# Kernel tuning notes

Hardware: AMD Instinct MI355X
Metric: run time of the kernel (lower is better)

Reference implementation:

```python
import jax, jax.numpy as jnp
import numpy as np

SUPPORT_FACTOR = 2.5
EPSILON = 1e-5


def setup_inputs() -> dict:
    key = jax.random.key(0)
    k1, _ = jax.random.split(key)
    # 64x64 regular particle grid on [0,1]^2 -> N = 4096 nodes
    n_side = 64
    g = jnp.linspace(0.0, 1.0, n_side, dtype=jnp.float32)
    gx, gy = jnp.meshgrid(g, g, indexing='ij')
    nodes = jnp.stack([gx.ravel(), gy.ravel()], axis=-1)  # [4096, 2]
    # B = 4096 query (collocation) points inside the same domain
    x = jax.random.uniform(k1, (4096, 2), dtype=jnp.float32)
    return {"x": x, "nodes": nodes}


def _cubic_spline(q):
    # piecewise cubic spline kernel; zero outside q > 1
    w_inner = 2.0 / 3.0 - 4.0 * q ** 2 + 4.0 * q ** 3          # q <= 0.5
    w_outer = 4.0 / 3.0 - 4.0 * q + 4.0 * q ** 2 - (4.0 / 3.0) * q ** 3  # 0.5 < q <= 1
    return jnp.where(q <= 0.5, w_inner, jnp.where(q <= 1.0, w_outer, 0.0))


def _dilation(nodes):
    # support_factor * mean nearest-neighbor spacing (replaces init-time cKDTree)
    d2 = jnp.sum((nodes[:, None, :] - nodes[None, :, :]) ** 2, axis=-1)  # [N, N]
    d2 = d2 + jnp.where(jnp.eye(nodes.shape[0], dtype=bool), jnp.inf, 0.0)
    h_avg = jnp.mean(jnp.sqrt(jnp.min(d2, axis=1)))
    return SUPPORT_FACTOR * h_avg


def reference(x, nodes):
    dilation = _dilation(nodes)
    diff = x[:, None, :] - nodes[None, :, :]          # [B, N, 2]
    dx = diff[..., 0]
    dy = diff[..., 1]
    dist = jnp.sqrt(dx ** 2 + dy ** 2 + 1e-10)        # [B, N]
    q = dist / dilation
    w = _cubic_spline(q) * (q <= 1.0)                 # support-radius mask
    ones = jnp.ones_like(dx)
    P = jnp.stack([ones, dx, dy], axis=-1)            # [B, N, 3]
    M = jnp.einsum('bni,bnj,bn->bij', P, P, w)        # [B, 3, 3] moment matrices
    M_reg = M + jnp.eye(3, dtype=x.dtype) * EPSILON
    M_inv = jnp.linalg.inv(M_reg)                     # batched 3x3 inverse
    P_w = P * w[..., None]
    b_vec = jnp.einsum('bij,bnj->bni', M_inv, P_w)    # [B, N, 3]
    phi = b_vec[..., 0]
    phi_x = -b_vec[..., 1]
    phi_y = -b_vec[..., 2]
    return (phi, phi_x, phi_y)
```

## Files before the change

### kernel.cpp

```cpp
#include <hip/hip_runtime.h>

#define N_NODES 4096
#define B_PTS   4096
#define SUPPORT_FACTOR 2.5f
#define EPSILON 1e-5f

__global__ __launch_bounds__(256) void nearest_kernel(
        const float* __restrict__ nodes, float* __restrict__ mind) {
    const int i = blockIdx.x;
    const float xi = nodes[2 * i];
    const float yi = nodes[2 * i + 1];

    const float4* nodes4 = (const float4*)nodes;
    float mind2 = 3.4e38f;
    for (int k = threadIdx.x; k < N_NODES / 2; k += 256) {
        float4 v = nodes4[k];
        float dx0 = xi - v.x, dy0 = yi - v.y;
        float dx1 = xi - v.z, dy1 = yi - v.w;
        float d20 = dx0 * dx0 + dy0 * dy0;
        float d21 = dx1 * dx1 + dy1 * dy1;
        if (2 * k != i)     mind2 = fminf(mind2, d20);
        if (2 * k + 1 != i) mind2 = fminf(mind2, d21);
    }
    #pragma unroll
    for (int off = 32; off > 0; off >>= 1)
        mind2 = fminf(mind2, __shfl_down(mind2, off, 64));

    __shared__ float sw[4];
    const int wave = threadIdx.x >> 6;
    if ((threadIdx.x & 63) == 0) sw[wave] = mind2;
    __syncthreads();
    if (threadIdx.x == 0) {
        float m = fminf(fminf(sw[0], sw[1]), fminf(sw[2], sw[3]));
        mind[i] = sqrtf(m);
    }
}

__device__ __forceinline__ float cubic_w(float q) {
    if (q <= 0.5f) return 2.0f / 3.0f + q * q * (4.0f * q - 4.0f);
    if (q <= 1.0f) return 4.0f / 3.0f + q * (-4.0f + q * (4.0f - (4.0f / 3.0f) * q));
    return 0.0f;
}

__global__ __launch_bounds__(256, 4) void rkpm_kernel(
        const float* __restrict__ x, const float* __restrict__ nodes,
        const float* __restrict__ mind, float* __restrict__ out) {
    __shared__ float sred[4][6];
    __shared__ float sbc[10];

    const int b = blockIdx.x;
    const int tid = threadIdx.x;
    const int wave = tid >> 6;
    const int lane = tid & 63;

    const float4* m4 = (const float4*)mind;
    float s = 0.f;
    #pragma unroll
    for (int k = 0; k < 4; ++k) {
        float4 v = m4[k * 256 + tid];
        s += (v.x + v.y) + (v.z + v.w);
    }
    #pragma unroll
    for (int off = 32; off > 0; off >>= 1)
        s += __shfl_down(s, off, 64);
    if (lane == 0) sred[wave][0] = s;
    __syncthreads();
    if (tid == 0) {
        float dil = (sred[0][0] + sred[1][0] + sred[2][0] + sred[3][0]) *
                    (SUPPORT_FACTOR / (float)N_NODES);
        sbc[0] = 1.0f / dil;
    }
    __syncthreads();
    const float inv_dil = sbc[0];

    const float2 xq = ((const float2*)x)[b];
    const float xb = xq.x, yb = xq.y;

    const float4* nodes4 = (const float4*)nodes;
    float wr[16], dxr[16], dyr[16];
    float m00 = 0.f, m01 = 0.f, m02 = 0.f, m11 = 0.f, m12 = 0.f, m22 = 0.f;
    #pragma unroll
    for (int kk = 0; kk < 4; ++kk) {
        float4 va = nodes4[kk * 512 + 2 * tid];
        float4 vb = nodes4[kk * 512 + 2 * tid + 1];
        #pragma unroll
        for (int c = 0; c < 4; ++c) {
            float nx = (c == 0) ? va.x : (c == 1) ? va.z : (c == 2) ? vb.x : vb.z;
            float ny = (c == 0) ? va.y : (c == 1) ? va.w : (c == 2) ? vb.y : vb.w;
            float dx = xb - nx;
            float dy = yb - ny;
            float dist = sqrtf(dx * dx + dy * dy + 1e-10f);
            float w = cubic_w(dist * inv_dil);
            const int r = kk * 4 + c;
            wr[r] = w; dxr[r] = dx; dyr[r] = dy;
            m00 += w;
            m01 += w * dx;
            m02 += w * dy;
            m11 += w * dx * dx;
            m12 += w * dx * dy;
            m22 += w * dy * dy;
        }
    }
    #pragma unroll
    for (int off = 32; off > 0; off >>= 1) {
        m00 += __shfl_down(m00, off, 64);
        m01 += __shfl_down(m01, off, 64);
        m02 += __shfl_down(m02, off, 64);
        m11 += __shfl_down(m11, off, 64);
        m12 += __shfl_down(m12, off, 64);
        m22 += __shfl_down(m22, off, 64);
    }
    if (lane == 0) {
        sred[wave][0] = m00; sred[wave][1] = m01; sred[wave][2] = m02;
        sred[wave][3] = m11; sred[wave][4] = m12; sred[wave][5] = m22;
    }
    __syncthreads();

    if (tid == 0) {
        float a  = sred[0][0] + sred[1][0] + sred[2][0] + sred[3][0] + EPSILON;
        float bb = sred[0][1] + sred[1][1] + sred[2][1] + sred[3][1];
        float c  = sred[0][2] + sred[1][2] + sred[2][2] + sred[3][2];
        float d  = sred[0][3] + sred[1][3] + sred[2][3] + sred[3][3] + EPSILON;
        float e  = sred[0][4] + sred[1][4] + sred[2][4] + sred[3][4];
        float f  = sred[0][5] + sred[1][5] + sred[2][5] + sred[3][5] + EPSILON;
        float c00 = d * f - e * e;
        float c01 = c * e - bb * f;
        float c02 = bb * e - c * d;
        float det = a * c00 + bb * c01 + c * c02;
        float idet = 1.0f / det;
        float i00 = c00 * idet;
        float i01 = c01 * idet;
        float i02 = c02 * idet;
        float i11 = (a * f - c * c) * idet;
        float i12 = (bb * c - a * e) * idet;
        float i22 = (a * d - bb * bb) * idet;
        sbc[1] = i00;  sbc[2] = i01;  sbc[3] = i02;
        sbc[4] = -i01; sbc[5] = -i11; sbc[6] = -i12;
        sbc[7] = -i02; sbc[8] = -i12; sbc[9] = -i22;
    }
    __syncthreads();

    const float i00 = sbc[1], i01 = sbc[2], i02 = sbc[3];
    const float n01 = sbc[4], n11 = sbc[5], n12 = sbc[6];
    const float n02 = sbc[7], n12b = sbc[8], n22 = sbc[9];

    const size_t BN = (size_t)B_PTS * N_NODES;
    float4* __restrict__ out_phi = (float4*)(out + (size_t)b * N_NODES);
    float4* __restrict__ out_px  = (float4*)(out + BN + (size_t)b * N_NODES);
    float4* __restrict__ out_py  = (float4*)(out + 2 * BN + (size_t)b * N_NODES);

    #pragma unroll
    for (int kk = 0; kk < 4; ++kk) {
        float4 ph, px, py;
        #pragma unroll
        for (int c = 0; c < 4; ++c) {
            const int r = kk * 4 + c;
            float w = wr[r], dx = dxr[r], dy = dyr[r];
            float vph = w * (i00 + i01 * dx + i02 * dy);
            float vpx = w * (n01 + n11 * dx + n12 * dy);
            float vpy = w * (n02 + n12b * dx + n22 * dy);
            if (c == 0)      { ph.x = vph; px.x = vpx; py.x = vpy; }
            else if (c == 1) { ph.y = vph; px.y = vpx; py.y = vpy; }
            else if (c == 2) { ph.z = vph; px.z = vpx; py.z = vpy; }
            else             { ph.w = vph; px.w = vpx; py.w = vpy; }
        }
        const int idx = kk * 256 + tid;
        out_phi[idx] = ph;
        out_px[idx]  = px;
        out_py[idx]  = py;
    }
}

extern "C" void kernel_launch(void* const* d_in, const int* in_sizes, int n_in,
                              void* d_out, int out_size, void* d_ws, size_t ws_size,
                              hipStream_t stream) {
    const float* x     = (const float*)d_in[0];
    const float* nodes = (const float*)d_in[1];
    float* out  = (float*)d_out;
    float* mind = (float*)d_ws;

    nearest_kernel<<<N_NODES, 256, 0, stream>>>(nodes, mind);
    rkpm_kernel<<<B_PTS, 256, 0, stream>>>(x, nodes, mind, out);
}
```

Measured before the change: 209.8 us.

## Exploit compact kernel support with zero-fill and sparse scatter of nonzeros

Each output row is first filled with zeros using float4 stores. Groups of four nodes are then culled by squared distance against the squared support radius, so the sqrt, spline and moment work run only for groups that can contribute. Surviving nonzero shape-function values are written with scalar scatter stores, and the register arrays that held all weights are gone. The dilation reduction moves into a single-block kernel, so the 4096 blocks no longer each re-read the whole nearest-distance buffer. The trade-off is a second pass over node positions, scalar stores that rewrite cache lines already zeroed, and one extra kernel launch.

```diff
diff --git a/kernel.cpp b/kernel.cpp
--- a/kernel.cpp
+++ b/kernel.cpp
@@ -36,69 +36,95 @@
     }
 }
 
+__global__ __launch_bounds__(256) void dil_kernel(float* __restrict__ mind) {
+    __shared__ float sw[4];
+    const int tid = threadIdx.x;
+    const float4* m4 = (const float4*)mind;
+    float s = 0.f;
+    #pragma unroll
+    for (int k = 0; k < 4; ++k) {
+        float4 v = m4[k * 256 + tid];
+        s += (v.x + v.y) + (v.z + v.w);
+    }
+    #pragma unroll
+    for (int off = 32; off > 0; off >>= 1)
+        s += __shfl_down(s, off, 64);
+    if ((tid & 63) == 0) sw[tid >> 6] = s;
+    __syncthreads();
+    if (tid == 0) {
+        float dil = (sw[0] + sw[1] + sw[2] + sw[3]) *
+                    (SUPPORT_FACTOR / (float)N_NODES);
+        mind[0] = 1.0f / dil;
+        mind[1] = dil * dil * 1.0002f + 1e-9f;
+    }
+}
+
 __device__ __forceinline__ float cubic_w(float q) {
     if (q <= 0.5f) return 2.0f / 3.0f + q * q * (4.0f * q - 4.0f);
     if (q <= 1.0f) return 4.0f / 3.0f + q * (-4.0f + q * (4.0f - (4.0f / 3.0f) * q));
     return 0.0f;
 }
 
-__global__ __launch_bounds__(256, 4) void rkpm_kernel(
+__global__ __launch_bounds__(256) void rkpm_sparse(
         const float* __restrict__ x, const float* __restrict__ nodes,
-        const float* __restrict__ mind, float* __restrict__ out) {
+        const float* __restrict__ dilp, float* __restrict__ out) {
     __shared__ float sred[4][6];
-    __shared__ float sbc[10];
+    __shared__ float sbc[9];
 
     const int b = blockIdx.x;
     const int tid = threadIdx.x;
     const int wave = tid >> 6;
     const int lane = tid & 63;
 
-    const float4* m4 = (const float4*)mind;
-    float s = 0.f;
-    #pragma unroll
-    for (int k = 0; k < 4; ++k) {
-        float4 v = m4[k * 256 + tid];
-        s += (v.x + v.y) + (v.z + v.w);
-    }
-    #pragma unroll
-    for (int off = 32; off > 0; off >>= 1)
-        s += __shfl_down(s, off, 64);
-    if (lane == 0) sred[wave][0] = s;
-    __syncthreads();
-    if (tid == 0) {
-        float dil = (sred[0][0] + sred[1][0] + sred[2][0] + sred[3][0]) *
-                    (SUPPORT_FACTOR / (float)N_NODES);
-        sbc[0] = 1.0f / dil;
-    }
-    __syncthreads();
-    const float inv_dil = sbc[0];
-
+    const size_t BN = (size_t)B_PTS * N_NODES;
+    float* __restrict__ row0 = out + (size_t)b * N_NODES;
+    float* __restrict__ row1 = row0 + BN;
+    float* __restrict__ row2 = row1 + BN;
+
+    {
+        float4 z4; z4.x = 0.f; z4.y = 0.f; z4.z = 0.f; z4.w = 0.f;
+        float4* p0 = (float4*)row0;
+        float4* p1 = (float4*)row1;
+        float4* p2 = (float4*)row2;
+        #pragma unroll
+        for (int k = 0; k < 4; ++k) {
+            p0[k * 256 + tid] = z4;
+            p1[k * 256 + tid] = z4;
+            p2[k * 256 + tid] = z4;
+        }
+    }
+
+    const float inv_dil = dilp[0];
+    const float r2m     = dilp[1];
     const float2 xq = ((const float2*)x)[b];
     const float xb = xq.x, yb = xq.y;
 
     const float4* nodes4 = (const float4*)nodes;
-    float wr[16], dxr[16], dyr[16];
     float m00 = 0.f, m01 = 0.f, m02 = 0.f, m11 = 0.f, m12 = 0.f, m22 = 0.f;
     #pragma unroll
     for (int kk = 0; kk < 4; ++kk) {
         float4 va = nodes4[kk * 512 + 2 * tid];
         float4 vb = nodes4[kk * 512 + 2 * tid + 1];
-        #pragma unroll
-        for (int c = 0; c < 4; ++c) {
-            float nx = (c == 0) ? va.x : (c == 1) ? va.z : (c == 2) ? vb.x : vb.z;
-            float ny = (c == 0) ? va.y : (c == 1) ? va.w : (c == 2) ? vb.y : vb.w;
-            float dx = xb - nx;
-            float dy = yb - ny;
-            float dist = sqrtf(dx * dx + dy * dy + 1e-10f);
-            float w = cubic_w(dist * inv_dil);
-            const int r = kk * 4 + c;
-            wr[r] = w; dxr[r] = dx; dyr[r] = dy;
-            m00 += w;
-            m01 += w * dx;
-            m02 += w * dy;
-            m11 += w * dx * dx;
-            m12 += w * dx * dy;
-            m22 += w * dy * dy;
+        float dx0 = xb - va.x, dy0 = yb - va.y;
+        float dx1 = xb - va.z, dy1 = yb - va.w;
+        float dx2 = xb - vb.x, dy2 = yb - vb.y;
+        float dx3 = xb - vb.z, dy3 = yb - vb.w;
+        float d0 = dx0 * dx0 + dy0 * dy0;
+        float d1 = dx1 * dx1 + dy1 * dy1;
+        float d2 = dx2 * dx2 + dy2 * dy2;
+        float d3 = dx3 * dx3 + dy3 * dy3;
+        float dmin = fminf(fminf(d0, d1), fminf(d2, d3));
+        if (dmin <= r2m) {
+            float w0 = cubic_w(sqrtf(d0 + 1e-10f) * inv_dil);
+            float w1 = cubic_w(sqrtf(d1 + 1e-10f) * inv_dil);
+            float w2 = cubic_w(sqrtf(d2 + 1e-10f) * inv_dil);
+            float w3 = cubic_w(sqrtf(d3 + 1e-10f) * inv_dil);
+            m00 += (w0 + w1) + (w2 + w3);
+            m01 += (w0 * dx0 + w1 * dx1) + (w2 * dx2 + w3 * dx3);
+            m02 += (w0 * dy0 + w1 * dy1) + (w2 * dy2 + w3 * dy3);
+            m11 += (w0 * dx0 * dx0 + w1 * dx1 * dx1) + (w2 * dx2 * dx2 + w3 * dx3 * dx3);
+            m12 += (w0 * dx0 * dy0 + w1 * dx1 * dy1) + (w2 * dx2 * dy2 + w3 * dx3 * dy3);
+            m22 += (w0 * dy0 * dy0 + w1 * dy1 * dy1) + (w2 * dy2 * dy2 + w3 * dy3 * dy3);
         }
     }
     #pragma unroll
@@ -134,41 +160,48 @@
         float i11 = (a * f - c * c) * idet;
         float i12 = (bb * c - a * e) * idet;
         float i22 = (a * d - bb * bb) * idet;
-        sbc[1] = i00;  sbc[2] = i01;  sbc[3] = i02;
-        sbc[4] = -i01; sbc[5] = -i11; sbc[6] = -i12;
-        sbc[7] = -i02; sbc[8] = -i12; sbc[9] = -i22;
-    }
-    __syncthreads();
-
-    const float i00 = sbc[1], i01 = sbc[2], i02 = sbc[3];
-    const float n01 = sbc[4], n11 = sbc[5], n12 = sbc[6];
-    const float n02 = sbc[7], n12b = sbc[8], n22 = sbc[9];
-
-    const size_t BN = (size_t)B_PTS * N_NODES;
-    float4* __restrict__ out_phi = (float4*)(out + (size_t)b * N_NODES);
-    float4* __restrict__ out_px  = (float4*)(out + BN + (size_t)b * N_NODES);
-    float4* __restrict__ out_py  = (float4*)(out + 2 * BN + (size_t)b * N_NODES);
+        sbc[0] = i00;  sbc[1] = i01;  sbc[2] = i02;
+        sbc[3] = -i01; sbc[4] = -i11; sbc[5] = -i12;
+        sbc[6] = -i02; sbc[7] = -i12; sbc[8] = -i22;
+    }
+    __syncthreads();
+
+    const float i00 = sbc[0], i01 = sbc[1], i02  = sbc[2];
+    const float n01 = sbc[3], n11 = sbc[4], n12  = sbc[5];
+    const float n02 = sbc[6], n12b = sbc[7], n22 = sbc[8];
+
+    #define SCATTER(DX, DY, DD, J)                                          \
+        {                                                                   \
+            float w_ = cubic_w(sqrtf((DD) + 1e-10f) * inv_dil);             \
+            if (w_ != 0.0f) {                                               \
+                row0[J] = w_ * (i00 + i01 * (DX) + i02  * (DY));            \
+                row1[J] = w_ * (n01 + n11 * (DX) + n12  * (DY));            \
+                row2[J] = w_ * (n02 + n12b * (DX) + n22 * (DY));            \
+            }                                                               \
+        }
 
     #pragma unroll
     for (int kk = 0; kk < 4; ++kk) {
-        float4 ph, px, py;
-        #pragma unroll
-        for (int c = 0; c < 4; ++c) {
-            const int r = kk * 4 + c;
-            float w = wr[r], dx = dxr[r], dy = dyr[r];
-            float vph = w * (i00 + i01 * dx + i02 * dy);
-            float vpx = w * (n01 + n11 * dx + n12 * dy);
-            float vpy = w * (n02 + n12b * dx + n22 * dy);
-            if (c == 0)      { ph.x = vph; px.x = vpx; py.x = vpy; }
-            else if (c == 1) { ph.y = vph; px.y = vpx; py.y = vpy; }
-            else if (c == 2) { ph.z = vph; px.z = vpx; py.z = vpy; }
-            else             { ph.w = vph; px.w = vpx; py.w = vpy; }
-        }
-        const int idx = kk * 256 + tid;
-        out_phi[idx] = ph;
-        out_px[idx]  = px;
-        out_py[idx]  = py;
-    }
+        float4 va = nodes4[kk * 512 + 2 * tid];
+        float4 vb = nodes4[kk * 512 + 2 * tid + 1];
+        float dx0 = xb - va.x, dy0 = yb - va.y;
+        float dx1 = xb - va.z, dy1 = yb - va.w;
+        float dx2 = xb - vb.x, dy2 = yb - vb.y;
+        float dx3 = xb - vb.z, dy3 = yb - vb.w;
+        float d0 = dx0 * dx0 + dy0 * dy0;
+        float d1 = dx1 * dx1 + dy1 * dy1;
+        float d2 = dx2 * dx2 + dy2 * dy2;
+        float d3 = dx3 * dx3 + dy3 * dy3;
+        float dmin = fminf(fminf(d0, d1), fminf(d2, d3));
+        if (dmin <= r2m) {
+            const int j = kk * 1024 + 4 * tid;
+            SCATTER(dx0, dy0, d0, j);
+            SCATTER(dx1, dy1, d1, j + 1);
+            SCATTER(dx2, dy2, d2, j + 2);
+            SCATTER(dx3, dy3, d3, j + 3);
+        }
+    }
+    #undef SCATTER
 }
 
 extern "C" void kernel_launch(void* const* d_in, const int* in_sizes, int n_in,
@@ -180,5 +213,6 @@
     float* mind = (float*)d_ws;
 
     nearest_kernel<<<N_NODES, 256, 0, stream>>>(nodes, mind);
-    rkpm_kernel<<<B_PTS, 256, 0, stream>>>(x, nodes, mind, out);
-}
+    dil_kernel<<<1, 256, 0, stream>>>(mind);
+    rkpm_sparse<<<B_PTS, 256, 0, stream>>>(x, nodes, mind, out);
+}
```

New measurement: 211.0 us. About the same (+0.5%).
